# Performance work log

Measured on AMD Instinct MI355X. Metric: run time of the kernel, lower is better.

## Reference

```python
import jax, jax.numpy as jnp
import numpy as np

TWO_PI = 2.0 * np.pi
PI = np.pi
RESONANCE_WEIGHT = 0.1


def setup_inputs() -> dict:
    key = jax.random.key(0)
    k1, k2, k3, k4, k5 = jax.random.split(key, 5)
    B, C = 16384, 1000          # batch, num classes for the CE term
    N, E = 4096, 131072         # graph nodes, directed edges (avg degree 32)
    outputs = jax.random.normal(k1, (B, C), dtype=jnp.float32)
    targets = jax.random.randint(k2, (B,), 0, C)
    resonance_phase = jax.random.normal(k3, (N, N), dtype=jnp.float32)
    edge_src = jax.random.randint(k4, (E,), 0, N)
    edge_dst = jax.random.randint(k5, (E,), 0, N)
    return {"outputs": outputs, "targets": targets,
            "resonance_phase": resonance_phase,
            "edge_src": edge_src, "edge_dst": edge_dst}


def reference(outputs, targets, resonance_phase, edge_src, edge_dst):
    # base_criterion: CrossEntropyLoss (mean reduction over batch)
    logp = jax.nn.log_softmax(outputs, axis=-1)                      # [B, C]
    base_loss = -jnp.mean(jnp.take_along_axis(logp, targets[:, None], axis=1))

    # resonance term: vectorized gather over all topology edges
    phase_ij = resonance_phase[edge_src, edge_dst]                   # [E]
    phase_ji = resonance_phase[edge_dst, edge_src]                   # [E]
    d = jnp.abs(phase_ij - phase_ji) % TWO_PI
    d = jnp.where(d > PI, TWO_PI - d, d)                             # wrap to [0, pi]
    resonance_loss = jnp.sum(d) / d.shape[0]                         # / total_connections

    return base_loss + RESONANCE_WEIGHT * resonance_loss
```

## Files before the change

### kernel.cpp

```cpp
#include <hip/hip_runtime.h>
#include <math.h>

#define TWO_PI_F 6.28318530717958647692f
#define PI_F     3.14159265358979323846f
#define CE_ROWS  4

typedef float f32x4 __attribute__((ext_vector_type(4)));

__device__ __forceinline__ float warp_sum(float s) {
    #pragma unroll
    for (int off = 32; off; off >>= 1) s += __shfl_xor(s, off, 64);
    return s;
}
__device__ __forceinline__ float warp_max(float m) {
    #pragma unroll
    for (int off = 32; off; off >>= 1) m = fmaxf(m, __shfl_xor(m, off, 64));
    return m;
}
__device__ __forceinline__ float max4(f32x4 v) {
    return fmaxf(fmaxf(v.x, v.y), fmaxf(v.z, v.w));
}

__device__ __forceinline__ float ce_compute(f32x4 v0, f32x4 v1, f32x4 v2, f32x4 v3,
                                            float tail, int t, int nf4, int remBase,
                                            int lane) {
    const int fj   = t >> 2;
    const int slot = t & 3;
    int owner;
    float cand;
    if (fj < nf4) {
        owner = fj & 63;
        const int reg = fj >> 6;
        f32x4 c4 = (reg == 0) ? v0 : (reg == 1) ? v1 : (reg == 2) ? v2 : v3;
        cand = (slot == 0) ? c4.x : (slot == 1) ? c4.y : (slot == 2) ? c4.z : c4.w;
    } else {
        owner = t - remBase;
        cand = tail;
    }
    const float tv = __shfl(cand, owner, 64);

    float m = tail;
    m = fmaxf(m, max4(v0));
    m = fmaxf(m, max4(v1));
    m = fmaxf(m, max4(v2));
    m = fmaxf(m, max4(v3));
    m = warp_max(m);

    float s;
    s  = __expf(v0.x - m) + __expf(v0.y - m) + __expf(v0.z - m) + __expf(v0.w - m);
    s += __expf(v1.x - m) + __expf(v1.y - m) + __expf(v1.z - m) + __expf(v1.w - m);
    s += __expf(v2.x - m) + __expf(v2.y - m) + __expf(v2.z - m) + __expf(v2.w - m);
    s += __expf(v3.x - m) + __expf(v3.y - m) + __expf(v3.z - m) + __expf(v3.w - m);
    s += __expf(tail - m);
    s = warp_sum(s);

    return m + __logf(s) - tv;
}

__device__ float ce_row_generic(const float* __restrict__ rowp, int C, int lane, int t) {
    const float4* row4 = (const float4*)rowp;
    const int nf4 = C >> 2;
    const float tv = rowp[t];
    float m = -INFINITY;
    for (int j = lane; j < nf4; j += 64) {
        float4 x = row4[j];
        m = fmaxf(m, fmaxf(fmaxf(x.x, x.y), fmaxf(x.z, x.w)));
    }
    const int remBase = nf4 << 2;
    if (remBase + lane < C) m = fmaxf(m, rowp[remBase + lane]);
    m = warp_max(m);
    float s = 0.0f;
    for (int j = lane; j < nf4; j += 64) {
        float4 x = row4[j];
        s += __expf(x.x - m) + __expf(x.y - m) + __expf(x.z - m) + __expf(x.w - m);
    }
    if (remBase + lane < C) s += __expf(rowp[remBase + lane] - m);
    s = warp_sum(s);
    return m + __logf(s) - tv;
}

#define LOAD_ROW(rowidx, V0, V1, V2, V3, VT)                                   \
    {                                                                          \
        const float* _p = outputs + (size_t)(rowidx) * (size_t)C;              \
        const f32x4* _q = (const f32x4*)_p;                                    \
        V0 = (j0 < nf4) ? __builtin_nontemporal_load(_q + j0) : NEG;           \
        V1 = (j1 < nf4) ? __builtin_nontemporal_load(_q + j1) : NEG;           \
        V2 = (j2 < nf4) ? __builtin_nontemporal_load(_q + j2) : NEG;           \
        V3 = (j3 < nf4) ? __builtin_nontemporal_load(_q + j3) : NEG;           \
        VT = (remBase + lane < C)                                              \
           ? __builtin_nontemporal_load(_p + remBase + lane) : -INFINITY;      \
    }

__global__ __launch_bounds__(256) void fused_kernel(
    const float* __restrict__ outputs,
    const int*   __restrict__ targets,
    const float* __restrict__ phase,
    const int*   __restrict__ esrc,
    const int*   __restrict__ edst,
    int B, int C, int N, int E,
    int res_blocks,
    float invB, float scaleE,
    float* __restrict__ ws)
{
    __shared__ float part[4];
    const int lane = threadIdx.x & 63;
    const int wave = threadIdx.x >> 6;

    float wsum = 0.0f;

    if ((int)blockIdx.x < res_blocks) {
        const int i = blockIdx.x * blockDim.x + threadIdx.x;
        float d = 0.0f;
        if (i < E) {
            const int s = esrc[i];
            const int t = edst[i];
            const float a = phase[(size_t)s * (size_t)N + (size_t)t];
            const float b = phase[(size_t)t * (size_t)N + (size_t)s];
            d = fabsf(a - b);
            d = fmodf(d, TWO_PI_F);
            if (d > PI_F) d = TWO_PI_F - d;
        }
        d = warp_sum(d);
        if (lane == 0) wsum = d * scaleE;
    } else {
        const int nf4 = C >> 2;
        const int wbase = (((int)blockIdx.x - res_blocks) * 4 + wave) * CE_ROWS;
        if (wbase < B) {
            if (nf4 <= 256 && wbase + CE_ROWS <= B) {
                const int remBase = nf4 << 2;
                const int j0 = lane, j1 = lane + 64, j2 = lane + 128, j3 = lane + 192;
                const f32x4 NEG = {-INFINITY, -INFINITY, -INFINITY, -INFINITY};

                const int4 t4 = *(const int4*)(targets + wbase);

                f32x4 a0, a1, a2, a3; float at;
                f32x4 b0, b1, b2, b3; float bt;
                f32x4 c0, c1, c2, c3; float ct;
                f32x4 d0, d1, d2, d3; float dt;
                LOAD_ROW(wbase + 0, a0, a1, a2, a3, at);
                LOAD_ROW(wbase + 1, b0, b1, b2, b3, bt);
                LOAD_ROW(wbase + 2, c0, c1, c2, c3, ct);
                LOAD_ROW(wbase + 3, d0, d1, d2, d3, dt);

                float acc;
                acc  = ce_compute(a0, a1, a2, a3, at, t4.x, nf4, remBase, lane);
                acc += ce_compute(b0, b1, b2, b3, bt, t4.y, nf4, remBase, lane);
                acc += ce_compute(c0, c1, c2, c3, ct, t4.z, nf4, remBase, lane);
                acc += ce_compute(d0, d1, d2, d3, dt, t4.w, nf4, remBase, lane);

                if (lane == 0) wsum = acc * invB;
            } else {
                float acc = 0.0f;
                for (int k = 0; k < CE_ROWS; ++k) {
                    const int row = wbase + k;
                    if (row < B)
                        acc += ce_row_generic(outputs + (size_t)row * (size_t)C,
                                              C, lane, targets[row]);
                }
                if (lane == 0) wsum = acc * invB;
            }
        }
    }

    if (lane == 0) part[wave] = wsum;
    __syncthreads();
    if (threadIdx.x == 0)
        ws[blockIdx.x] = part[0] + part[1] + part[2] + part[3];
}

__global__ __launch_bounds__(512) void reduce_kernel(
    const float* __restrict__ ws, int P, float* __restrict__ out)
{
    float s = 0.0f;
    for (int i = threadIdx.x; i < P; i += 512)
        s += ws[i];
    s = warp_sum(s);
    __shared__ float part[8];
    if ((threadIdx.x & 63) == 0) part[threadIdx.x >> 6] = s;
    __syncthreads();
    if (threadIdx.x == 0) {
        float tot = 0.0f;
        #pragma unroll
        for (int i = 0; i < 8; i++) tot += part[i];
        out[0] = tot;
    }
}

extern "C" void kernel_launch(void* const* d_in, const int* in_sizes, int n_in,
                              void* d_out, int out_size, void* d_ws, size_t ws_size,
                              hipStream_t stream) {
    const float* outputs = (const float*)d_in[0];
    const int*   targets = (const int*)d_in[1];
    const float* phase   = (const float*)d_in[2];
    const int*   esrc    = (const int*)d_in[3];
    const int*   edst    = (const int*)d_in[4];

    const int B = in_sizes[1];
    const int C = in_sizes[0] / B;
    const int E = in_sizes[3];
    int N = 1;
    while ((long long)N * (long long)N < (long long)in_sizes[2]) N++;

    const int res_blocks = (E + 255) / 256;
    const int rows_per_block = 4 * CE_ROWS;
    const int ce_blocks  = (B + rows_per_block - 1) / rows_per_block;
    const int grid = res_blocks + ce_blocks;

    float* ws = (float*)d_ws;

    fused_kernel<<<grid, 256, 0, stream>>>(outputs, targets, phase, esrc, edst,
                                           B, C, N, E, res_blocks,
                                           1.0f / (float)B, 0.1f / (float)E,
                                           ws);
    reduce_kernel<<<1, 512, 0, stream>>>(ws, grid, (float*)d_out);
}
```

Measured before the change: 141.9 us.

## Interleave edge gathers into cross-entropy blocks so they overlap with row loads

```diff
diff --git a/kernel.cpp b/kernel.cpp
--- a/kernel.cpp
+++ b/kernel.cpp
@@ -98,7 +98,6 @@
     const int*   __restrict__ esrc,
     const int*   __restrict__ edst,
     int B, int C, int N, int E,
-    int res_blocks,
     float invB, float scaleE,
     float* __restrict__ ws)
 {
@@ -106,60 +105,87 @@
     const int lane = threadIdx.x & 63;
     const int wave = threadIdx.x >> 6;
 
+    const int gi = blockIdx.x * blockDim.x + threadIdx.x;
+    const bool has_edge = gi < (E << 1);
+    int es = 0, ed = 0;
+    if (has_edge) {
+        const int e = gi >> 1;
+        es = esrc[e];
+        ed = edst[e];
+    }
+
+    const int nf4 = C >> 2;
+    const int wbase = (blockIdx.x * 4 + wave) * CE_ROWS;
     float wsum = 0.0f;
 
-    if ((int)blockIdx.x < res_blocks) {
-        const int i = blockIdx.x * blockDim.x + threadIdx.x;
-        float d = 0.0f;
-        if (i < E) {
-            const int s = esrc[i];
-            const int t = edst[i];
-            const float a = phase[(size_t)s * (size_t)N + (size_t)t];
-            const float b = phase[(size_t)t * (size_t)N + (size_t)s];
-            d = fabsf(a - b);
-            d = fmodf(d, TWO_PI_F);
-            if (d > PI_F) d = TWO_PI_F - d;
-        }
-        d = warp_sum(d);
-        if (lane == 0) wsum = d * scaleE;
+    if (nf4 <= 256 && wbase + CE_ROWS <= B) {
+        const int remBase = nf4 << 2;
+        const int j0 = lane, j1 = lane + 64, j2 = lane + 128, j3 = lane + 192;
+        const f32x4 NEG = {-INFINITY, -INFINITY, -INFINITY, -INFINITY};
+
+        const int4 t4 = *(const int4*)(targets + wbase);
+
+        f32x4 a0, a1, a2, a3; float at;
+        f32x4 b0, b1, b2, b3; float bt;
+        f32x4 c0, c1, c2, c3; float ct;
+        f32x4 d0, d1, d2, d3; float dt;
+        LOAD_ROW(wbase + 0, a0, a1, a2, a3, at);
+        LOAD_ROW(wbase + 1, b0, b1, b2, b3, bt);
+        LOAD_ROW(wbase + 2, c0, c1, c2, c3, ct);
+        LOAD_ROW(wbase + 3, d0, d1, d2, d3, dt);
+
+        float pv = 0.0f;
+        if (has_edge) {
+            const int r = (gi & 1) ? ed : es;
+            const int c = (gi & 1) ? es : ed;
+            pv = phase[(size_t)r * (size_t)N + (size_t)c];
+        }
+
+        float acc;
+        acc  = ce_compute(a0, a1, a2, a3, at, t4.x, nf4, remBase, lane);
+        acc += ce_compute(b0, b1, b2, b3, bt, t4.y, nf4, remBase, lane);
+        acc += ce_compute(c0, c1, c2, c3, ct, t4.z, nf4, remBase, lane);
+        acc += ce_compute(d0, d1, d2, d3, dt, t4.w, nf4, remBase, lane);
+
+        float dterm = 0.0f;
+        if (has_edge) {
+            const float other = __shfl_xor(pv, 1, 64);
+            if (!(gi & 1)) {
+                float dd = fabsf(pv - other);
+                dd = fmodf(dd, TWO_PI_F);
+                if (dd > PI_F) dd = TWO_PI_F - dd;
+                dterm = dd;
+            }
+        }
+        const float esum = warp_sum(dterm);
+        if (lane == 0) wsum = acc * invB + esum * scaleE;
     } else {
-        const int nf4 = C >> 2;
-        const int wbase = (((int)blockIdx.x - res_blocks) * 4 + wave) * CE_ROWS;
-        if (wbase < B) {
-            if (nf4 <= 256 && wbase + CE_ROWS <= B) {
-                const int remBase = nf4 << 2;
-                const int j0 = lane, j1 = lane + 64, j2 = lane + 128, j3 = lane + 192;
-                const f32x4 NEG = {-INFINITY, -INFINITY, -INFINITY, -INFINITY};
-
-                const int4 t4 = *(const int4*)(targets + wbase);
-
-                f32x4 a0, a1, a2, a3; float at;
-                f32x4 b0, b1, b2, b3; float bt;
-                f32x4 c0, c1, c2, c3; float ct;
-                f32x4 d0, d1, d2, d3; float dt;
-                LOAD_ROW(wbase + 0, a0, a1, a2, a3, at);
-                LOAD_ROW(wbase + 1, b0, b1, b2, b3, bt);
-                LOAD_ROW(wbase + 2, c0, c1, c2, c3, ct);
-                LOAD_ROW(wbase + 3, d0, d1, d2, d3, dt);
-
-                float acc;
-                acc  = ce_compute(a0, a1, a2, a3, at, t4.x, nf4, remBase, lane);
-                acc += ce_compute(b0, b1, b2, b3, bt, t4.y, nf4, remBase, lane);
-                acc += ce_compute(c0, c1, c2, c3, ct, t4.z, nf4, remBase, lane);
-                acc += ce_compute(d0, d1, d2, d3, dt, t4.w, nf4, remBase, lane);
-
-                if (lane == 0) wsum = acc * invB;
-            } else {
-                float acc = 0.0f;
-                for (int k = 0; k < CE_ROWS; ++k) {
-                    const int row = wbase + k;
-                    if (row < B)
-                        acc += ce_row_generic(outputs + (size_t)row * (size_t)C,
-                                              C, lane, targets[row]);
-                }
-                if (lane == 0) wsum = acc * invB;
+        float pv = 0.0f;
+        if (has_edge) {
+            const int r = (gi & 1) ? ed : es;
+            const int c = (gi & 1) ? es : ed;
+            pv = phase[(size_t)r * (size_t)N + (size_t)c];
+        }
+        float dterm = 0.0f;
+        if (has_edge) {
+            const float other = __shfl_xor(pv, 1, 64);
+            if (!(gi & 1)) {
+                float dd = fabsf(pv - other);
+                dd = fmodf(dd, TWO_PI_F);
+                if (dd > PI_F) dd = TWO_PI_F - dd;
+                dterm = dd;
             }
         }
+        const float esum = warp_sum(dterm);
+
+        float acc = 0.0f;
+        for (int k = 0; k < CE_ROWS; ++k) {
+            const int row = wbase + k;
+            if (row < B)
+                acc += ce_row_generic(outputs + (size_t)row * (size_t)C,
+                                      C, lane, targets[row]);
+        }
+        if (lane == 0) wsum = acc * invB + esum * scaleE;
     }
 
     if (lane == 0) part[wave] = wsum;
@@ -201,15 +227,15 @@
     int N = 1;
     while ((long long)N * (long long)N < (long long)in_sizes[2]) N++;
 
-    const int res_blocks = (E + 255) / 256;
     const int rows_per_block = 4 * CE_ROWS;
-    const int ce_blocks  = (B + rows_per_block - 1) / rows_per_block;
-    const int grid = res_blocks + ce_blocks;
+    const int ce_blocks   = (B + rows_per_block - 1) / rows_per_block;
+    const int edge_blocks = (2 * E + 255) / 256;
+    const int grid = (ce_blocks > edge_blocks) ? ce_blocks : edge_blocks;
 
     float* ws = (float*)d_ws;
 
     fused_kernel<<<grid, 256, 0, stream>>>(outputs, targets, phase, esrc, edst,
-                                           B, C, N, E, res_blocks,
+                                           B, C, N, E,
                                            1.0f / (float)B, 0.1f / (float)E,
                                            ws);
     reduce_kernel<<<1, 512, 0, stream>>>(ws, grid, (float*)d_out);
```

Result: no change. 143.8 us (+1.4%).
